# Kernel optimization log

Measured on AMD Instinct MI355X. Metric: run time of the kernel, lower is better.

## Reference

```python
import jax, jax.numpy as jnp
import numpy as np
import math

H = 16
D_MODEL = 1024
D_K = D_MODEL // H


def setup_inputs() -> dict:
    key = jax.random.key(0)
    ks = jax.random.split(key, 11)
    B, S, D = 4, 2048, D_MODEL
    scale = 1.0 / math.sqrt(D)
    inp = {
        "query": jax.random.normal(ks[0], (B, S, D), jnp.float32),
        "key": jax.random.normal(ks[1], (B, S, D), jnp.float32),
        "value": jax.random.normal(ks[2], (B, S, D), jnp.float32),
        # four Linear(d_model, d_model) layers: Wq, Wk, Wv, Wo (weights stored [in, out])
        "Wq": jax.random.normal(ks[3], (D, D), jnp.float32) * scale,
        "bq": jnp.zeros((D,), jnp.float32),
        "Wk": jax.random.normal(ks[4], (D, D), jnp.float32) * scale,
        "bk": jnp.zeros((D,), jnp.float32),
        "Wv": jax.random.normal(ks[5], (D, D), jnp.float32) * scale,
        "bv": jnp.zeros((D,), jnp.float32),
        "Wo": jax.random.normal(ks[6], (D, D), jnp.float32) * scale,
        "bo": jnp.zeros((D,), jnp.float32),
    }
    return inp


def reference(query, key, value, Wq, bq, Wk, bk, Wv, bv, Wo, bo):
    B, S, D = query.shape
    # QKV projections, split into heads: [B, H, S, d_k]
    def proj(x, W, b):
        return (x @ W + b).reshape(B, -1, H, D_K).transpose(0, 2, 1, 3)

    q = proj(query, Wq, bq)
    k = proj(key, Wk, bk)
    v = proj(value, Wv, bv)

    # scaled dot-product attention (mask=None, dropout p=0 -> identity)
    scores = jnp.einsum("bhqd,bhkd->bhqk", q, k) / math.sqrt(D_K)
    p_attn = jax.nn.softmax(scores, axis=-1)
    x = jnp.einsum("bhqk,bhkd->bhqd", p_attn, v)

    # merge heads and output projection
    x = x.transpose(0, 2, 1, 3).reshape(B, -1, H * D_K)
    return x @ Wo + bo
```

## Files before the change

kernel.cpp:

```cpp
#include <hip/hip_runtime.h>


typedef unsigned short u16;
typedef unsigned int u32;
typedef __attribute__((ext_vector_type(8))) short bfx8;
typedef __attribute__((ext_vector_type(4))) float f32x4;
typedef __attribute__((ext_vector_type(4))) float fx4;
typedef __attribute__((ext_vector_type(8))) u16 u16x8;
typedef __attribute__((ext_vector_type(4))) u16 u16x4;
typedef __attribute__((ext_vector_type(2))) u32 u32x2;

__device__ __forceinline__ u16 f2bf(float f) {
  union { float f; u32 u; } v; v.f = f;
  u32 u = v.u;
  u += 0x7fffu + ((u >> 16) & 1u);
  return (u16)(u >> 16);
}

__device__ __forceinline__ u32 cvtpk(float a, float b) {
  u32 r;
  asm("v_cvt_pk_bf16_f32 %0, %1, %2" : "=v"(r) : "v"(a), "v"(b));
  return r;
}

__device__ __forceinline__ void gl_lds16(const void* g, void* l) {
  __builtin_amdgcn_global_load_lds((const __attribute__((address_space(1))) void*)g,
                                   (__attribute__((address_space(3))) void*)l, 16, 0, 0);
}

__global__ void prep(const float* __restrict__ q, const float* __restrict__ k,
                     const float* __restrict__ v, u16* __restrict__ inBase,
                     const float* __restrict__ W0, const float* __restrict__ W1,
                     const float* __restrict__ W2, const float* __restrict__ W3,
                     u16* __restrict__ WtBase) {
  __shared__ float tile[64][65];
  const int bid = blockIdx.x;
  const int t = threadIdx.x;
  if (bid < 12288) {
    const int z = bid >> 12, xb = bid & 4095;
    const float* in = z == 0 ? q : (z == 1 ? k : v);
    u16* out = inBase + (size_t)z * (8192ull * 1024);
    const int i = (xb * 256 + t) * 8;
    fx4 a = *(const fx4*)(in + i);
    fx4 b = *(const fx4*)(in + i + 4);
    u16x8 o;
    o[0] = f2bf(a[0]); o[1] = f2bf(a[1]); o[2] = f2bf(a[2]); o[3] = f2bf(a[3]);
    o[4] = f2bf(b[0]); o[5] = f2bf(b[1]); o[6] = f2bf(b[2]); o[7] = f2bf(b[3]);
    *(u16x8*)(out + i) = o;
  } else {
    const int wb = bid - 12288;
    const int z = wb >> 8, rem = wb & 255;
    const float* W = z == 0 ? W0 : (z == 1 ? W1 : (z == 2 ? W2 : W3));
    u16* Wt = WtBase + (size_t)z * (1024ull * 1024);
    const int n0 = (rem & 15) << 6, k0 = (rem >> 4) << 6;
    {
      int r = t >> 2, c = (t & 3) << 4;
      const float* src = W + (size_t)(k0 + r) * 1024 + n0 + c;
#pragma unroll
      for (int u = 0; u < 4; ++u) {
        fx4 vv = *(const fx4*)(src + u * 4);
        tile[r][c + u * 4 + 0] = vv[0];
        tile[r][c + u * 4 + 1] = vv[1];
        tile[r][c + u * 4 + 2] = vv[2];
        tile[r][c + u * 4 + 3] = vv[3];
      }
    }
    __syncthreads();
    {
      int nn = t >> 2, j = t & 3;
      u16x8 o0, o1;
#pragma unroll
      for (int e = 0; e < 8; ++e) o0[e] = f2bf(tile[(j << 4) + e][nn]);
#pragma unroll
      for (int e = 0; e < 8; ++e) o1[e] = f2bf(tile[(j << 4) + 8 + e][nn]);
      u16* dst = Wt + (size_t)(n0 + nn) * 1024 + k0 + (j << 4);
      *(u16x8*)dst = o0;
      *(u16x8*)(dst + 8) = o1;
    }
  }
}

template <int EPI>
__device__ __forceinline__ void gemm_body(const u16* __restrict__ A, const u16* __restrict__ Bt,
                                          const float* __restrict__ bias, void* __restrict__ out,
                                          float scale, char* smem, int m0, int n0) {
  const int t = threadIdx.x;
  const int w = t >> 6, l = t & 63;
  const int lg = l >> 4, lr = l & 15;
  const int wr = w >> 1, wc = w & 1;

  f32x4 acc[4][4] = {};

  const int trow = t >> 3;
  const int scb = ((t & 7) << 4) ^ ((trow & 7) << 4);
  const char* gA = (const char*)A + (size_t)(m0 + trow) * 2048;
  const char* gB = (const char*)Bt + (size_t)(n0 + trow) * 2048;

#define GSTAGE(kt, buf)                                                        \
  do {                                                                         \
    _Pragma("unroll")                                                          \
    for (int i = 0; i < 4; ++i) {                                              \
      gl_lds16(gA + (size_t)i * 32 * 2048 + ((kt) << 7) + scb,                 \
               (buf) + (((i << 8) + (w << 6)) << 4));                          \
      gl_lds16(gB + (size_t)i * 32 * 2048 + ((kt) << 7) + scb,                 \
               (buf) + 16384 + (((i << 8) + (w << 6)) << 4));                  \
    }                                                                          \
  } while (0)

  GSTAGE(0, smem);
  __syncthreads();

  for (int kt = 0; kt < 16; ++kt) {
    char* sA = smem + ((kt & 1) << 15);
    char* sB = sA + 16384;
    if (kt < 15) GSTAGE(kt + 1, smem + (((kt + 1) & 1) << 15));

#pragma unroll
    for (int kk = 0; kk < 2; ++kk) {
      const int off = ((kk << 6) + (lg << 4)) ^ ((lr & 7) << 4);
      bfx8 av[4], bv[4];
#pragma unroll
      for (int fi = 0; fi < 4; ++fi)
        av[fi] = *(const bfx8*)(sA + ((wr << 6) + (fi << 4) + lr) * 128 + off);
#pragma unroll
      for (int fj = 0; fj < 4; ++fj)
        bv[fj] = *(const bfx8*)(sB + ((wc << 6) + (fj << 4) + lr) * 128 + off);
#pragma unroll
      for (int fi = 0; fi < 4; ++fi)
#pragma unroll
        for (int fj = 0; fj < 4; ++fj)
          acc[fi][fj] = __builtin_amdgcn_mfma_f32_16x16x32_bf16(av[fi], bv[fj], acc[fi][fj], 0, 0, 0);
    }
    __syncthreads();
  }
#undef GSTAGE

#pragma unroll
  for (int fj = 0; fj < 4; ++fj) {
    const int n = n0 + (wc << 6) + (fj << 4) + lr;
    const float bvl = bias[n];
#pragma unroll
    for (int fi = 0; fi < 4; ++fi) {
      if constexpr (EPI == 2) {
        const int h = n >> 6, d = n & 63;
        const int mm = m0 + (wr << 6) + (fi << 4) + (lg << 2);
        const int b = mm >> 11, s = mm & 2047;
        u16x4 pk4;
#pragma unroll
        for (int r = 0; r < 4; ++r) pk4[r] = f2bf(acc[fi][fj][r] + bvl);
        *(u16x4*)((u16*)out + (size_t)(b * 16 + h) * 131072 + (size_t)d * 2048 + s) = pk4;
      } else {
#pragma unroll
        for (int r = 0; r < 4; ++r) {
          const int m = m0 + (wr << 6) + (fi << 4) + (lg << 2) + r;
          const float val = (acc[fi][fj][r] + bvl) * scale;
          if constexpr (EPI == 0) {
            const int b = m >> 11, s = m & 2047, h = n >> 6, d = n & 63;
            ((u16*)out)[(((size_t)(b * 16 + h) * 2048 + s) << 6) + d] = f2bf(val);
          } else {
            ((float*)out)[((size_t)m << 10) + n] = val;
          }
        }
      }
    }
  }
}

__device__ __forceinline__ void xcd_remap(int& m0, int& n0) {
  const int lin = blockIdx.x + (blockIdx.y << 3);
  const int c = lin & 7, j = lin >> 3;
  m0 = (((j & 7) << 3) + c) << 7;
  n0 = (j >> 3) << 7;
}

__global__ void __launch_bounds__(256, 2)
gemm_qkv(const u16* __restrict__ A0, const u16* __restrict__ Wt0,
         const float* __restrict__ bq, const float* __restrict__ bk,
         const float* __restrict__ bv, u16* __restrict__ out0, u16* __restrict__ vt) {
  __shared__ __align__(16) char smem[65536];
  const int z = blockIdx.z;
  int m0, n0;
  xcd_remap(m0, n0);
  const u16* A = A0 + (size_t)z * (8192ull * 1024);
  const u16* Bt = Wt0 + (size_t)z * (1024ull * 1024);
  if (z == 2) {
    gemm_body<2>(A, Bt, bv, vt, 1.0f, smem, m0, n0);
  } else {
    const float* bias = z == 0 ? bq : bk;
    const float scale = z == 0 ? 0.18033688011112042f : 1.0f;
    gemm_body<0>(A, Bt, bias, out0 + (size_t)z * (8192ull * 1024), scale, smem, m0, n0);
  }
}

__global__ void __launch_bounds__(256, 2)
gemm_o(const u16* __restrict__ A, const u16* __restrict__ Bt,
       const float* __restrict__ bias, float* __restrict__ out) {
  __shared__ __align__(16) char smem[65536];
  int m0, n0;
  xcd_remap(m0, n0);
  gemm_body<1>(A, Bt, bias, out, 1.0f, smem, m0, n0);
}

__global__ void __launch_bounds__(512, 4)
attn_fwd(const u16* __restrict__ Qg, const u16* __restrict__ Kg,
         const u16* __restrict__ Vtg, u16* __restrict__ Og) {
  __shared__ __align__(16) char smem[65536];
  const int t = threadIdx.x;
  const int w = t >> 6, l = t & 63;
  const int lg = l >> 4, lr = l & 15;

  const int id = blockIdx.x;
  const int xcd = id & 7, slot = id >> 3;
  const int pair = ((slot >> 3) << 3) + xcd;
  const int q0 = (slot & 7) << 8;

  const char* Qb = (const char*)Qg + ((size_t)pair << 18);
  const char* Kb = (const char*)Kg + ((size_t)pair << 18);
  const char* Vb = (const char*)Vtg + ((size_t)pair << 18);
  char* sPw = smem + 32768 + (w << 12);

  const int trow = t >> 3;
  const int scb = ((t & 7) << 4) ^ ((trow & 7) << 4);
  const int ldst = (w << 10);

  bfx8 qf[2][2];
#pragma unroll
  for (int fi = 0; fi < 2; ++fi)
#pragma unroll
    for (int kk = 0; kk < 2; ++kk)
      qf[fi][kk] = *(const bfx8*)(Qb + (size_t)(q0 + (w << 5) + (fi << 4) + lr) * 128 +
                                  (kk << 6) + (lg << 4));

  f32x4 accO[2][4] = {};
  float Lp[2] = {0.f, 0.f};
  const int sw0 = (lr & 7) << 4;

#define ASTAGE(kt, buf)                                                         \
  do {                                                                          \
    gl_lds16(Kb + (size_t)(kt) * 8192 + (size_t)trow * 128 + scb, (buf) + ldst);\
    gl_lds16(Vb + (size_t)trow * 4096 + (size_t)(kt) * 128 + scb,               \
             (buf) + 8192 + ldst);                                              \
  } while (0)

  ASTAGE(0, smem);
  __syncthreads();

  for (int it = 0; it < 32; ++it) {
    char* bK = smem + ((it & 1) << 14);
    char* bV = bK + 8192;
    if (it < 31) ASTAGE(it + 1, smem + (((it + 1) & 1) << 14));

    f32x4 accS[2][4] = {};
    __builtin_amdgcn_s_setprio(1);
#pragma unroll
    for (int kk = 0; kk < 2; ++kk) {
      const int off = ((kk << 6) + (lg << 4)) ^ sw0;
      bfx8 kf[4];
#pragma unroll
      for (int fj = 0; fj < 4; ++fj)
        kf[fj] = *(const bfx8*)(bK + (((fj << 4) + lr) << 7) + off);
#pragma unroll
      for (int fi = 0; fi < 2; ++fi)
#pragma unroll
        for (int fj = 0; fj < 4; ++fj)
          accS[fi][fj] = __builtin_amdgcn_mfma_f32_16x16x32_bf16(kf[fj], qf[fi][kk], accS[fi][fj], 0, 0, 0);
    }
    __builtin_amdgcn_s_setprio(0);

#pragma unroll
    for (int fi = 0; fi < 2; ++fi) {
      char* prow = sPw + (((fi << 4) + lr) << 7);
#pragma unroll
      for (int fj = 0; fj < 4; ++fj) {
        const float p0 = __builtin_amdgcn_exp2f(accS[fi][fj][0]);
        const float p1 = __builtin_amdgcn_exp2f(accS[fi][fj][1]);
        const float p2 = __builtin_amdgcn_exp2f(accS[fi][fj][2]);
        const float p3 = __builtin_amdgcn_exp2f(accS[fi][fj][3]);
        Lp[fi] += (p0 + p1) + (p2 + p3);
        u32x2 pk;
        pk[0] = cvtpk(p0, p1);
        pk[1] = cvtpk(p2, p3);
        *(u32x2*)(prow + (((fj << 5) + (lg << 3)) ^ sw0)) = pk;
      }
    }

    __builtin_amdgcn_s_setprio(1);
#pragma unroll
    for (int kk = 0; kk < 2; ++kk) {
      const int off = ((kk << 6) + (lg << 4)) ^ sw0;
      bfx8 pf[2], vf[4];
#pragma unroll
      for (int fi = 0; fi < 2; ++fi)
        pf[fi] = *(const bfx8*)(sPw + (((fi << 4) + lr) << 7) + off);
#pragma unroll
      for (int dj = 0; dj < 4; ++dj)
        vf[dj] = *(const bfx8*)(bV + (((dj << 4) + lr) << 7) + off);
#pragma unroll
      for (int fi = 0; fi < 2; ++fi)
#pragma unroll
        for (int dj = 0; dj < 4; ++dj)
          accO[fi][dj] = __builtin_amdgcn_mfma_f32_16x16x32_bf16(pf[fi], vf[dj], accO[fi][dj], 0, 0, 0);
    }
    __builtin_amdgcn_s_setprio(0);

    __syncthreads();
  }
#undef ASTAGE

  __builtin_amdgcn_sched_barrier(0);
  float* Lbuf = (float*)sPw;
#pragma unroll
  for (int fi = 0; fi < 2; ++fi)
    Lbuf[(lg << 5) + (fi << 4) + lr] = Lp[fi];

  float rinv[2][4];
#pragma unroll
  for (int fi = 0; fi < 2; ++fi)
#pragma unroll
    for (int r = 0; r < 4; ++r) {
      const int qrow = (fi << 4) + (lg << 2) + r;
      float s = Lbuf[qrow] + Lbuf[32 + qrow] + Lbuf[64 + qrow] + Lbuf[96 + qrow];
      rinv[fi][r] = 1.0f / s;
    }
  __builtin_amdgcn_sched_barrier(0);

  const int b = pair >> 4, h = pair & 15;
#pragma unroll
  for (int fi = 0; fi < 2; ++fi) {
    u16* bb = (u16*)sPw;
#pragma unroll
    for (int dj = 0; dj < 4; ++dj)
#pragma unroll
      for (int r = 0; r < 4; ++r)
        bb[((lg << 2) + r) * 72 + (dj << 4) + lr] = f2bf(accO[fi][dj][r] * rinv[fi][r]);

    const int rrow = l >> 2, rc = (l & 3) << 4;
    u16x8 o0 = *(const u16x8*)(bb + rrow * 72 + rc);
    u16x8 o1 = *(const u16x8*)(bb + rrow * 72 + rc + 8);
    const int srow = q0 + (w << 5) + (fi << 4) + rrow;
    u16* dst = Og + (((size_t)(b * 2048 + srow)) << 10) + (h << 6) + rc;
    *(u16x8*)dst = o0;
    *(u16x8*)(dst + 8) = o1;
  }
}

extern "C" void kernel_launch(void* const* d_in, const int* in_sizes, int n_in,
                              void* d_out, int out_size, void* d_ws, size_t ws_size,
                              hipStream_t stream) {
  const float* q  = (const float*)d_in[0];
  const float* k  = (const float*)d_in[1];
  const float* v  = (const float*)d_in[2];
  const float* Wq = (const float*)d_in[3];
  const float* bq = (const float*)d_in[4];
  const float* Wk = (const float*)d_in[5];
  const float* bk = (const float*)d_in[6];
  const float* Wv = (const float*)d_in[7];
  const float* bv = (const float*)d_in[8];
  const float* Wo = (const float*)d_in[9];
  const float* bo = (const float*)d_in[10];
  float* out = (float*)d_out;
  char* ws = (char*)d_ws;

  const size_t MB = 1024 * 1024;
  if (ws_size < 104 * MB) return;

  u16* inq = (u16*)(ws + 0 * MB);
  u16* wqt = (u16*)(ws + 48 * MB);
  u16* wot = (u16*)(ws + 54 * MB);
  u16* Qh  = (u16*)(ws + 56 * MB);
  u16* Kh  = (u16*)(ws + 72 * MB);
  u16* Vth = (u16*)(ws + 88 * MB);
  u16* Ob  = inq;

  prep<<<13312, 256, 0, stream>>>(q, k, v, inq, Wq, Wk, Wv, Wo, wqt);
  gemm_qkv<<<dim3(8, 64, 3), 256, 0, stream>>>(inq, wqt, bq, bk, bv, Qh, Vth);
  attn_fwd<<<512, 512, 0, stream>>>(Qh, Kh, Vth, Ob);
  gemm_o<<<dim3(8, 64), 256, 0, stream>>>(Ob, wot, bo, out);
}
```

Measured before the change: 186.9 us.

## Switch attention to 32x32x16 MFMA and keep P in registers via permlane swap

Rewrites the attention inner loop to use 32x32x16 bf16 MFMA tiles instead of 16x16x32. The S accumulator layout is rearranged with v_permlane32_swap so the exponentiated probabilities feed the PV MFMA straight from registers, which removes the per-wave LDS round trip for P and shrinks shared memory from 64 KiB to about 33 KiB. The epilogue now combines row sums with a shuffle and writes scalar bf16 stores. This risks higher register pressure from the 16-wide accumulators, and the narrower output stores may coalesce worse.

```diff
diff --git a/kernel.cpp b/kernel.cpp
--- a/kernel.cpp
+++ b/kernel.cpp
@@ -5,10 +5,11 @@
 typedef unsigned int u32;
 typedef __attribute__((ext_vector_type(8))) short bfx8;
 typedef __attribute__((ext_vector_type(4))) float f32x4;
+typedef __attribute__((ext_vector_type(16))) float f32x16;
 typedef __attribute__((ext_vector_type(4))) float fx4;
 typedef __attribute__((ext_vector_type(8))) u16 u16x8;
 typedef __attribute__((ext_vector_type(4))) u16 u16x4;
-typedef __attribute__((ext_vector_type(2))) u32 u32x2;
+typedef __attribute__((ext_vector_type(4))) u32 u32x4;
 
 __device__ __forceinline__ u16 f2bf(float f) {
   union { float f; u32 u; } v; v.f = f;
@@ -204,10 +205,10 @@
 __global__ void __launch_bounds__(512, 4)
 attn_fwd(const u16* __restrict__ Qg, const u16* __restrict__ Kg,
          const u16* __restrict__ Vtg, u16* __restrict__ Og) {
-  __shared__ __align__(16) char smem[65536];
+  __shared__ __align__(16) char smem[33792];
   const int t = threadIdx.x;
   const int w = t >> 6, l = t & 63;
-  const int lg = l >> 4, lr = l & 15;
+  const int l31 = l & 31, hi = l >> 5;
 
   const int id = blockIdx.x;
   const int xcd = id & 7, slot = id >> 3;
@@ -217,23 +218,19 @@
   const char* Qb = (const char*)Qg + ((size_t)pair << 18);
   const char* Kb = (const char*)Kg + ((size_t)pair << 18);
   const char* Vb = (const char*)Vtg + ((size_t)pair << 18);
-  char* sPw = smem + 32768 + (w << 12);
 
   const int trow = t >> 3;
   const int scb = ((t & 7) << 4) ^ ((trow & 7) << 4);
   const int ldst = (w << 10);
-
-  bfx8 qf[2][2];
-#pragma unroll
-  for (int fi = 0; fi < 2; ++fi)
-#pragma unroll
-    for (int kk = 0; kk < 2; ++kk)
-      qf[fi][kk] = *(const bfx8*)(Qb + (size_t)(q0 + (w << 5) + (fi << 4) + lr) * 128 +
-                                  (kk << 6) + (lg << 4));
-
-  f32x4 accO[2][4] = {};
-  float Lp[2] = {0.f, 0.f};
-  const int sw0 = (lr & 7) << 4;
+  const int swz = (l & 7) << 4;
+
+  bfx8 qf[4];
+#pragma unroll
+  for (int ks = 0; ks < 4; ++ks)
+    qf[ks] = *(const bfx8*)(Qb + (size_t)(q0 + (w << 5) + l31) * 128 + (ks << 5) + (hi << 4));
+
+  f32x16 accO[2] = {};
+  float Lp = 0.f;
 
 #define ASTAGE(kt, buf)                                                         \
   do {                                                                          \
@@ -250,56 +247,48 @@
     char* bV = bK + 8192;
     if (it < 31) ASTAGE(it + 1, smem + (((it + 1) & 1) << 14));
 
-    f32x4 accS[2][4] = {};
+    f32x16 accS[2] = {{}, {}};
     __builtin_amdgcn_s_setprio(1);
 #pragma unroll
-    for (int kk = 0; kk < 2; ++kk) {
-      const int off = ((kk << 6) + (lg << 4)) ^ sw0;
+    for (int mb = 0; mb < 2; ++mb) {
       bfx8 kf[4];
 #pragma unroll
-      for (int fj = 0; fj < 4; ++fj)
-        kf[fj] = *(const bfx8*)(bK + (((fj << 4) + lr) << 7) + off);
-#pragma unroll
-      for (int fi = 0; fi < 2; ++fi)
-#pragma unroll
-        for (int fj = 0; fj < 4; ++fj)
-          accS[fi][fj] = __builtin_amdgcn_mfma_f32_16x16x32_bf16(kf[fj], qf[fi][kk], accS[fi][fj], 0, 0, 0);
+      for (int ks = 0; ks < 4; ++ks)
+        kf[ks] = *(const bfx8*)(bK + (((mb << 5) + l31) << 7) + (((ks << 5) + (hi << 4)) ^ swz));
+#pragma unroll
+      for (int ks = 0; ks < 4; ++ks)
+        accS[mb] = __builtin_amdgcn_mfma_f32_32x32x16_bf16(kf[ks], qf[ks], accS[mb], 0, 0, 0);
     }
     __builtin_amdgcn_s_setprio(0);
 
-#pragma unroll
-    for (int fi = 0; fi < 2; ++fi) {
-      char* prow = sPw + (((fi << 4) + lr) << 7);
-#pragma unroll
-      for (int fj = 0; fj < 4; ++fj) {
-        const float p0 = __builtin_amdgcn_exp2f(accS[fi][fj][0]);
-        const float p1 = __builtin_amdgcn_exp2f(accS[fi][fj][1]);
-        const float p2 = __builtin_amdgcn_exp2f(accS[fi][fj][2]);
-        const float p3 = __builtin_amdgcn_exp2f(accS[fi][fj][3]);
-        Lp[fi] += (p0 + p1) + (p2 + p3);
-        u32x2 pk;
-        pk[0] = cvtpk(p0, p1);
-        pk[1] = cvtpk(p2, p3);
-        *(u32x2*)(prow + (((fj << 5) + (lg << 3)) ^ sw0)) = pk;
+    bfx8 pa[4];
+#pragma unroll
+    for (int mb = 0; mb < 2; ++mb) {
+#pragma unroll
+      for (int r = 0; r < 16; ++r) {
+        accS[mb][r] = __builtin_amdgcn_exp2f(accS[mb][r]);
+        Lp += accS[mb][r];
       }
+#pragma unroll
+      for (int half = 0; half < 2; ++half) {
+        u32 a0 = cvtpk(accS[mb][8 * half + 0], accS[mb][8 * half + 1]);
+        u32 a1 = cvtpk(accS[mb][8 * half + 2], accS[mb][8 * half + 3]);
+        u32 b0 = cvtpk(accS[mb][8 * half + 4], accS[mb][8 * half + 5]);
+        u32 b1 = cvtpk(accS[mb][8 * half + 6], accS[mb][8 * half + 7]);
+        asm volatile("v_permlane32_swap_b32 %0, %1" : "+v"(a0), "+v"(b0));
+        asm volatile("v_permlane32_swap_b32 %0, %1" : "+v"(a1), "+v"(b1));
+        u32x4 pk; pk[0] = a0; pk[1] = a1; pk[2] = b0; pk[3] = b1;
+        pa[(mb << 1) + half] = *(bfx8*)&pk;
+      }
     }
 
     __builtin_amdgcn_s_setprio(1);
 #pragma unroll
-    for (int kk = 0; kk < 2; ++kk) {
-      const int off = ((kk << 6) + (lg << 4)) ^ sw0;
-      bfx8 pf[2], vf[4];
-#pragma unroll
-      for (int fi = 0; fi < 2; ++fi)
-        pf[fi] = *(const bfx8*)(sPw + (((fi << 4) + lr) << 7) + off);
-#pragma unroll
-      for (int dj = 0; dj < 4; ++dj)
-        vf[dj] = *(const bfx8*)(bV + (((dj << 4) + lr) << 7) + off);
-#pragma unroll
-      for (int fi = 0; fi < 2; ++fi)
-#pragma unroll
-        for (int dj = 0; dj < 4; ++dj)
-          accO[fi][dj] = __builtin_amdgcn_mfma_f32_16x16x32_bf16(pf[fi], vf[dj], accO[fi][dj], 0, 0, 0);
+    for (int ks = 0; ks < 4; ++ks) {
+      bfx8 vf0 = *(const bfx8*)(bV + ((0 + l31) << 7) + (((ks << 5) + (hi << 4)) ^ swz));
+      bfx8 vf1 = *(const bfx8*)(bV + ((32 + l31) << 7) + (((ks << 5) + (hi << 4)) ^ swz));
+      accO[0] = __builtin_amdgcn_mfma_f32_32x32x16_bf16(pa[ks], vf0, accO[0], 0, 0, 0);
+      accO[1] = __builtin_amdgcn_mfma_f32_32x32x16_bf16(pa[ks], vf1, accO[1], 0, 0, 0);
     }
     __builtin_amdgcn_s_setprio(0);
 
@@ -307,40 +296,19 @@
   }
 #undef ASTAGE
 
-  __builtin_amdgcn_sched_barrier(0);
-  float* Lbuf = (float*)sPw;
-#pragma unroll
-  for (int fi = 0; fi < 2; ++fi)
-    Lbuf[(lg << 5) + (fi << 4) + lr] = Lp[fi];
-
-  float rinv[2][4];
-#pragma unroll
-  for (int fi = 0; fi < 2; ++fi)
-#pragma unroll
-    for (int r = 0; r < 4; ++r) {
-      const int qrow = (fi << 4) + (lg << 2) + r;
-      float s = Lbuf[qrow] + Lbuf[32 + qrow] + Lbuf[64 + qrow] + Lbuf[96 + qrow];
-      rinv[fi][r] = 1.0f / s;
-    }
-  __builtin_amdgcn_sched_barrier(0);
-
+  const float Ltot = Lp + __shfl_xor(Lp, 32);
+  float* Lb = (float*)(smem + 32768) + (w << 5);
+  if (l < 32) Lb[l31] = Ltot;
+  __builtin_amdgcn_s_waitcnt(0);
   const int b = pair >> 4, h = pair & 15;
-#pragma unroll
-  for (int fi = 0; fi < 2; ++fi) {
-    u16* bb = (u16*)sPw;
-#pragma unroll
-    for (int dj = 0; dj < 4; ++dj)
-#pragma unroll
-      for (int r = 0; r < 4; ++r)
-        bb[((lg << 2) + r) * 72 + (dj << 4) + lr] = f2bf(accO[fi][dj][r] * rinv[fi][r]);
-
-    const int rrow = l >> 2, rc = (l & 3) << 4;
-    u16x8 o0 = *(const u16x8*)(bb + rrow * 72 + rc);
-    u16x8 o1 = *(const u16x8*)(bb + rrow * 72 + rc + 8);
-    const int srow = q0 + (w << 5) + (fi << 4) + rrow;
-    u16* dst = Og + (((size_t)(b * 2048 + srow)) << 10) + (h << 6) + rc;
-    *(u16x8*)dst = o0;
-    *(u16x8*)(dst + 8) = o1;
+  u16* dstBase = Og + (((size_t)(b * 2048 + q0 + (w << 5))) << 10) + (h << 6) + l31;
+#pragma unroll
+  for (int r = 0; r < 16; ++r) {
+    const int ql = (r & 3) + ((r >> 2) << 3) + (hi << 2);
+    const float rinv = __builtin_amdgcn_rcpf(Lb[ql]);
+    u16* dst = dstBase + ((size_t)ql << 10);
+    dst[0]  = f2bf(accO[0][r] * rinv);
+    dst[32] = f2bf(accO[1][r] * rinv);
   }
 }
 
```

Measured after the change: 185.1 us. No clear change (-0.9%).
